# Optimization experiments

Measured on AMD Instinct MI355X. Metric: run time of the kernel, lower is better.

Reference implementation:

```python
import jax, jax.numpy as jnp
import numpy as np

B, N, NIN, NH, NOUT = 32, 64, 256, 256, 2
E = N * (N - 1)
BN_EPS = 1e-5


def _xavier(k, fan_in, fan_out):
    return jax.random.normal(k, (fan_in, fan_out), jnp.float32) * np.sqrt(2.0 / (fan_in + fan_out))


def _mlp_params(key, n_in, n_hid, n_out):
    k1, k2 = jax.random.split(key)
    return {
        'w1': _xavier(k1, n_in, n_hid), 'b1': jnp.full((n_hid,), 0.1, jnp.float32),
        'w2': _xavier(k2, n_hid, n_out), 'b2': jnp.full((n_out,), 0.1, jnp.float32),
        'g': jnp.ones((n_out,), jnp.float32), 'beta': jnp.zeros((n_out,), jnp.float32),
    }


def setup_inputs() -> dict:
    key = jax.random.key(0)
    ks = jax.random.split(key, 7)
    inputs = jax.random.normal(ks[0], (B, N, NIN), jnp.float32)
    # fully-connected directed graph w/o self loops: edge e = (send i, recv j), i != j
    idx = np.array([(i, j) for i in range(N) for j in range(N) if i != j], dtype=np.int64)
    rel_send = np.zeros((E, N), np.float32)
    rel_rec = np.zeros((E, N), np.float32)
    rel_send[np.arange(E), idx[:, 0]] = 1.0
    rel_rec[np.arange(E), idx[:, 1]] = 1.0
    out = {'inputs': inputs, 'rel_rec': jnp.asarray(rel_rec), 'rel_send': jnp.asarray(rel_send)}
    for name, (ni, nh, no), k in [('mlp1', (NIN, NH, NH), ks[1]),
                                  ('mlp2', (2 * NH, NH, NH), ks[2]),
                                  ('mlp3', (NH, NH, NH), ks[3]),
                                  ('mlp4', (3 * NH, NH, NH), ks[4])]:
        p = _mlp_params(k, ni, nh, no)
        for pk, pv in p.items():
            out[f'{name}_{pk}'] = pv
    out['fc_w'] = _xavier(ks[5], NH, NOUT)
    out['fc_b'] = jnp.full((NOUT,), 0.1, jnp.float32)
    return out


def _mlp(x, w1, b1, w2, b2, g, beta):
    # Linear -> ELU -> Linear -> ELU -> BatchNorm1d (training-mode batch stats, biased var)
    h = jax.nn.elu(x @ w1 + b1)
    h = jax.nn.elu(h @ w2 + b2)
    mean = h.mean(axis=(0, 1))
    var = h.var(axis=(0, 1))
    return (h - mean) * jax.lax.rsqrt(var + BN_EPS) * g + beta


def reference(inputs, rel_rec, rel_send,
              mlp1_w1, mlp1_b1, mlp1_w2, mlp1_b2, mlp1_g, mlp1_beta,
              mlp2_w1, mlp2_b1, mlp2_w2, mlp2_b2, mlp2_g, mlp2_beta,
              mlp3_w1, mlp3_b1, mlp3_w2, mlp3_b2, mlp3_g, mlp3_beta,
              mlp4_w1, mlp4_b1, mlp4_w2, mlp4_b2, mlp4_g, mlp4_beta,
              fc_w, fc_b):
    x = _mlp(inputs, mlp1_w1, mlp1_b1, mlp1_w2, mlp1_b2, mlp1_g, mlp1_beta)  # [B,N,NH]
    # node2edge: gather sender/receiver node features per edge
    s = jnp.einsum('en,bnh->beh', rel_send, x)
    r = jnp.einsum('en,bnh->beh', rel_rec, x)
    x = jnp.concatenate([s, r], axis=-1)  # [B,E,2*NH]
    x = _mlp(x, mlp2_w1, mlp2_b1, mlp2_w2, mlp2_b2, mlp2_g, mlp2_beta)
    x_skip = x
    # edge2node: scatter-sum incoming edges per node, normalized by N
    inc = jnp.einsum('en,beh->bnh', rel_rec, x) / N
    x = _mlp(inc, mlp3_w1, mlp3_b1, mlp3_w2, mlp3_b2, mlp3_g, mlp3_beta)
    s = jnp.einsum('en,bnh->beh', rel_send, x)
    r = jnp.einsum('en,bnh->beh', rel_rec, x)
    x = jnp.concatenate([s, r, x_skip], axis=-1)  # [B,E,3*NH]
    x = _mlp(x, mlp4_w1, mlp4_b1, mlp4_w2, mlp4_b2, mlp4_g, mlp4_beta)
    return x @ fc_w + fc_b  # [B,E,NOUT]
```

## Files before the change

kernel.cpp:

```cpp
#include <hip/hip_runtime.h>

typedef __bf16 bf16_t;
typedef __bf16 bf16x8 __attribute__((ext_vector_type(8)));
typedef float  f32x4  __attribute__((ext_vector_type(4)));

#define NB    64
#define EB    4032
#define BATCH 32
#define H     256
#define M_EDGE (BATCH*EB)
#define M_NODE (BATCH*NB)
#define T2    4
#define T4    4
#define BN_EPS 1e-5f

__device__ __forceinline__ void load_lds16(const void* g, void* l) {
    __builtin_amdgcn_global_load_lds(
        (const __attribute__((address_space(1))) unsigned int*)g,
        (__attribute__((address_space(3))) unsigned int*)l, 16, 0, 0);
}
__device__ __forceinline__ float elu(float v) { return v > 0.f ? v : __expf(v) - 1.f; }

template<bool AF32>
__global__ __launch_bounds__(256)
void fused_mlp(const void* __restrict__ A0v,
               const bf16_t* __restrict__ W1t, const float* __restrict__ b1,
               const bf16_t* __restrict__ W2t, const float* __restrict__ b2,
               bf16_t* __restrict__ out, float* __restrict__ stats)
{
    const int m0 = blockIdx.x * 64;
    const int tid = threadIdx.x, wave = tid >> 6, lane = tid & 63;
    const int l15 = lane & 15, quad = lane >> 4;
    const int row = tid >> 2;
    const int cx8 = (((tid & 3) ^ ((tid >> 3) & 3))) * 8;
    const int sl8 = (tid & 3) * 8;
    const int xq8 = (quad ^ ((l15 >> 1) & 3)) * 8;

    __shared__ bf16_t h1s[64 * 264];
    __shared__ bf16_t Bs[256 * 32];
    __shared__ float  sred[512];

    const bf16_t* A0 = (const bf16_t*)A0v;

    f32x4 acc1[4][4];
#pragma unroll
    for (int t = 0; t < 4; ++t)
#pragma unroll
        for (int u = 0; u < 4; ++u) acc1[t][u] = (f32x4){0.f, 0.f, 0.f, 0.f};

    for (int k0 = 0; k0 < 256; k0 += 32) {
        bf16_t* ldsA = h1s + wave * 512;
        if (AF32) {
            const float* af = (const float*)A0v + (size_t)(m0 + row) * 256 + k0 + cx8;
            float4 lo = *(const float4*)af;
            float4 hi = *(const float4*)(af + 4);
            bf16x8 v;
            v[0]=(bf16_t)lo.x; v[1]=(bf16_t)lo.y; v[2]=(bf16_t)lo.z; v[3]=(bf16_t)lo.w;
            v[4]=(bf16_t)hi.x; v[5]=(bf16_t)hi.y; v[6]=(bf16_t)hi.z; v[7]=(bf16_t)hi.w;
            *(bf16x8*)&h1s[row * 32 + sl8] = v;
        } else {
            load_lds16(A0 + (size_t)(m0 + row) * 256 + k0 + cx8, ldsA);
        }
#pragma unroll
        for (int p = 0; p < 4; ++p)
            load_lds16(W1t + (size_t)(p * 64 + row) * 256 + k0 + cx8,
                       Bs + (p * 256 + wave * 64) * 8);
        __syncthreads();
        bf16x8 afr[4], bfr[4];
#pragma unroll
        for (int t = 0; t < 4; ++t)
            afr[t] = *(const bf16x8*)&h1s[(t * 16 + l15) * 32 + xq8];
#pragma unroll
        for (int u = 0; u < 4; ++u)
            bfr[u] = *(const bf16x8*)&Bs[(wave * 64 + u * 16 + l15) * 32 + xq8];
#pragma unroll
        for (int t = 0; t < 4; ++t)
#pragma unroll
            for (int u = 0; u < 4; ++u)
                acc1[t][u] = __builtin_amdgcn_mfma_f32_16x16x32_bf16(afr[t], bfr[u], acc1[t][u], 0, 0, 0);
        __syncthreads();
    }

#pragma unroll
    for (int u = 0; u < 4; ++u) {
        int   col = wave * 64 + u * 16 + l15;
        float bv  = b1[col];
#pragma unroll
        for (int t = 0; t < 4; ++t)
#pragma unroll
            for (int r = 0; r < 4; ++r)
                h1s[(t * 16 + quad * 4 + r) * 264 + col] = (bf16_t)elu(acc1[t][u][r] + bv);
    }
    sred[tid] = 0.f; sred[256 + tid] = 0.f;
    __syncthreads();

    f32x4 acc2[4][4];
#pragma unroll
    for (int t = 0; t < 4; ++t)
#pragma unroll
        for (int u = 0; u < 4; ++u) acc2[t][u] = (f32x4){0.f, 0.f, 0.f, 0.f};

    for (int k0 = 0; k0 < 256; k0 += 32) {
#pragma unroll
        for (int p = 0; p < 4; ++p)
            load_lds16(W2t + (size_t)(p * 64 + row) * 256 + k0 + cx8,
                       Bs + (p * 256 + wave * 64) * 8);
        __syncthreads();
        bf16x8 afr[4], bfr[4];
#pragma unroll
        for (int t = 0; t < 4; ++t)
            afr[t] = *(const bf16x8*)&h1s[(t * 16 + l15) * 264 + k0 + quad * 8];
#pragma unroll
        for (int u = 0; u < 4; ++u)
            bfr[u] = *(const bf16x8*)&Bs[(wave * 64 + u * 16 + l15) * 32 + xq8];
#pragma unroll
        for (int t = 0; t < 4; ++t)
#pragma unroll
            for (int u = 0; u < 4; ++u)
                acc2[t][u] = __builtin_amdgcn_mfma_f32_16x16x32_bf16(afr[t], bfr[u], acc2[t][u], 0, 0, 0);
        __syncthreads();
    }

#pragma unroll
    for (int u = 0; u < 4; ++u) {
        int   col = wave * 64 + u * 16 + l15;
        float bv  = b2[col];
        float s = 0.f, q = 0.f;
#pragma unroll
        for (int t = 0; t < 4; ++t)
#pragma unroll
            for (int r = 0; r < 4; ++r) {
                float v = elu(acc2[t][u][r] + bv);
                h1s[(t * 16 + quad * 4 + r) * 264 + col] = (bf16_t)v;
                s += v; q += v * v;
            }
        s += __shfl_xor(s, 16); s += __shfl_xor(s, 32);
        q += __shfl_xor(q, 16); q += __shfl_xor(q, 32);
        if (quad == 0) { atomicAdd(&sred[col], s); atomicAdd(&sred[256 + col], q); }
    }
    __syncthreads();
#pragma unroll
    for (int p = 0; p < 8; ++p) {
        int idx = p * 256 + tid;
        int r = idx >> 5, ch = idx & 31;
        *(uint4*)&out[(size_t)(m0 + r) * H + ch * 8] = *(const uint4*)&h1s[r * 264 + ch * 8];
    }
    atomicAdd(&stats[tid],     sred[tid]);
    atomicAdd(&stats[H + tid], sred[256 + tid]);
}

__global__ __launch_bounds__(256)
void node_gemm(const bf16_t* __restrict__ A, const float* __restrict__ statsIn,
               const float* __restrict__ g, const float* __restrict__ beta, float Mcnt,
               const bf16_t* __restrict__ Wt, const float* __restrict__ bias,
               float* __restrict__ out)
{
    const int m0 = blockIdx.x * 64;
    const int nb = blockIdx.y * 256;
    const int tid = threadIdx.x, wave = tid >> 6, lane = tid & 63;
    const int l15 = lane & 15, quad = lane >> 4;
    const int row = tid >> 2;
    const int cx8 = (((tid & 3) ^ ((tid >> 3) & 3))) * 8;
    const int sl8 = (tid & 3) * 8;
    const int xq8 = (quad ^ ((l15 >> 1) & 3)) * 8;
    __shared__ bf16_t As[64 * 32];
    __shared__ bf16_t Bs[256 * 32];
    __shared__ float  ss[512];

    {
        float mean = statsIn[tid] / Mcnt;
        float var  = statsIn[256 + tid] / Mcnt - mean * mean;
        float scl  = g[tid] * rsqrtf(var + BN_EPS);
        ss[tid]       = scl;
        ss[256 + tid] = beta[tid] - mean * scl;
    }
    __syncthreads();

    f32x4 acc[4][4];
#pragma unroll
    for (int t = 0; t < 4; ++t)
#pragma unroll
        for (int u = 0; u < 4; ++u) acc[t][u] = (f32x4){0.f, 0.f, 0.f, 0.f};

    for (int k0 = 0; k0 < 256; k0 += 32) {
        {
            int kc = k0 + cx8;
            bf16x8 v = *(const bf16x8*)(A + (size_t)(m0 + row) * 256 + kc);
            bf16x8 w;
#pragma unroll
            for (int j = 0; j < 8; ++j)
                w[j] = (bf16_t)((float)v[j] * ss[kc + j] + ss[256 + kc + j]);
            *(bf16x8*)&As[row * 32 + sl8] = w;
        }
#pragma unroll
        for (int p = 0; p < 4; ++p)
            load_lds16(Wt + (size_t)(nb + p * 64 + row) * 256 + k0 + cx8,
                       Bs + (p * 256 + wave * 64) * 8);
        __syncthreads();
        bf16x8 afr[4], bfr[4];
#pragma unroll
        for (int t = 0; t < 4; ++t)
            afr[t] = *(const bf16x8*)&As[(t * 16 + l15) * 32 + xq8];
#pragma unroll
        for (int u = 0; u < 4; ++u)
            bfr[u] = *(const bf16x8*)&Bs[(wave * 64 + u * 16 + l15) * 32 + xq8];
#pragma unroll
        for (int t = 0; t < 4; ++t)
#pragma unroll
            for (int u = 0; u < 4; ++u)
                acc[t][u] = __builtin_amdgcn_mfma_f32_16x16x32_bf16(afr[t], bfr[u], acc[t][u], 0, 0, 0);
        __syncthreads();
    }
#pragma unroll
    for (int u = 0; u < 4; ++u) {
        int col = nb + wave * 64 + u * 16 + l15;
        float bv = bias[col];
#pragma unroll
        for (int t = 0; t < 4; ++t)
#pragma unroll
            for (int r = 0; r < 4; ++r)
                out[(size_t)(m0 + t * 16 + quad * 4 + r) * 512 + col] = acc[t][u][r] + bv;
    }
}

__global__ __launch_bounds__(256, 2)
void m2_kernel(const float* __restrict__ PQ, const bf16_t* __restrict__ W2t,
               const float* __restrict__ b2, bf16_t* __restrict__ out,
               float* __restrict__ stats)
{
    const int tile0 = blockIdx.x * T2;
    const int tid = threadIdx.x, wave = tid >> 6, lane = tid & 63;
    const int l15 = lane & 15, quad = lane >> 4;

    __shared__ bf16_t Abuf[2][64 * 264];
    __shared__ float  sred[512];

    bf16x8 Breg[32];
#pragma unroll
    for (int ks = 0; ks < 8; ++ks)
#pragma unroll
        for (int u = 0; u < 4; ++u) {
            int col = wave * 64 + u * 16 + l15;
            Breg[ks * 4 + u] = *(const bf16x8*)(W2t + (size_t)col * 256 + ks * 32 + quad * 8);
        }
    sred[tid] = 0.f; sred[256 + tid] = 0.f;

    auto computeA = [&](int t, int b) {
        int row = tid >> 2;
        int m = (tile0 + t) * 64 + row;
        int bb = m / EB, e = m - bb * EB;
        int sn = e / (NB - 1), rr = e - sn * (NB - 1);
        int rc = rr + (rr >= sn ? 1 : 0);
        const float* Prow = PQ + (size_t)(bb * NB + sn) * 512;
        const float* Qrow = PQ + (size_t)(bb * NB + rc) * 512 + 256;
        int c0 = (tid & 3) * 64;
#pragma unroll
        for (int j = 0; j < 8; ++j) {
            int c = c0 + j * 8;
            float4 p0 = *(const float4*)(Prow + c);
            float4 p1 = *(const float4*)(Prow + c + 4);
            float4 q0 = *(const float4*)(Qrow + c);
            float4 q1 = *(const float4*)(Qrow + c + 4);
            bf16x8 v;
            v[0]=(bf16_t)elu(p0.x+q0.x); v[1]=(bf16_t)elu(p0.y+q0.y);
            v[2]=(bf16_t)elu(p0.z+q0.z); v[3]=(bf16_t)elu(p0.w+q0.w);
            v[4]=(bf16_t)elu(p1.x+q1.x); v[5]=(bf16_t)elu(p1.y+q1.y);
            v[6]=(bf16_t)elu(p1.z+q1.z); v[7]=(bf16_t)elu(p1.w+q1.w);
            *(bf16x8*)&Abuf[b][row * 264 + c] = v;
        }
    };

    computeA(0, 0);
    __syncthreads();

    for (int t = 0; t < T2; ++t) {
        const int cur = t & 1, nxt = cur ^ 1;
        if (t + 1 < T2) computeA(t + 1, nxt);

        f32x4 acc[4][4];
#pragma unroll
        for (int a = 0; a < 4; ++a)
#pragma unroll
            for (int u = 0; u < 4; ++u) acc[a][u] = (f32x4){0.f, 0.f, 0.f, 0.f};
#pragma unroll
        for (int ks = 0; ks < 8; ++ks) {
            bf16x8 afr[4];
#pragma unroll
            for (int a = 0; a < 4; ++a)
                afr[a] = *(const bf16x8*)&Abuf[cur][(a * 16 + l15) * 264 + ks * 32 + quad * 8];
#pragma unroll
            for (int a = 0; a < 4; ++a)
#pragma unroll
                for (int u = 0; u < 4; ++u)
                    acc[a][u] = __builtin_amdgcn_mfma_f32_16x16x32_bf16(afr[a], Breg[ks * 4 + u], acc[a][u], 0, 0, 0);
        }
        __syncthreads();

#pragma unroll
        for (int u = 0; u < 4; ++u) {
            int   col = wave * 64 + u * 16 + l15;
            float bv  = b2[col];
            float s = 0.f, q = 0.f;
#pragma unroll
            for (int a = 0; a < 4; ++a)
#pragma unroll
                for (int r = 0; r < 4; ++r) {
                    float v = elu(acc[a][u][r] + bv);
                    Abuf[cur][(a * 16 + quad * 4 + r) * 264 + col] = (bf16_t)v;
                    s += v; q += v * v;
                }
            s += __shfl_xor(s, 16); s += __shfl_xor(s, 32);
            q += __shfl_xor(q, 16); q += __shfl_xor(q, 32);
            if (quad == 0) { atomicAdd(&sred[col], s); atomicAdd(&sred[256 + col], q); }
        }
        __syncthreads();

        size_t m0 = (size_t)(tile0 + t) * 64;
#pragma unroll
        for (int p = 0; p < 8; ++p) {
            int idx = p * 256 + tid;
            int r = idx >> 5, ch = idx & 31;
            *(uint4*)&out[(m0 + r) * H + ch * 8] = *(const uint4*)&Abuf[cur][r * 264 + ch * 8];
        }
        __syncthreads();
    }
    atomicAdd(&stats[tid],     sred[tid]);
    atomicAdd(&stats[H + tid], sred[256 + tid]);
}

__global__ __launch_bounds__(256, 1)
void m4_kernel(const bf16_t* __restrict__ h2, const bf16_t* __restrict__ Wskt,
               const float* __restrict__ RS, const bf16_t* __restrict__ W2t,
               const float* __restrict__ b2, bf16_t* __restrict__ out,
               float* __restrict__ stats)
{
    const int tile0 = blockIdx.x * T4;
    const int tid = threadIdx.x, wave = tid >> 6, lane = tid & 63;
    const int l15 = lane & 15, quad = lane >> 4;

    __shared__ bf16_t Abuf[2][64 * 264];
    __shared__ float  sred[512];

    bf16x8 B1r[32], B2r[32];
#pragma unroll
    for (int ks = 0; ks < 8; ++ks)
#pragma unroll
        for (int u = 0; u < 4; ++u) {
            int col = wave * 64 + u * 16 + l15;
            B1r[ks * 4 + u] = *(const bf16x8*)(Wskt + (size_t)col * 256 + ks * 32 + quad * 8);
            B2r[ks * 4 + u] = *(const bf16x8*)(W2t  + (size_t)col * 256 + ks * 32 + quad * 8);
        }
    sred[tid] = 0.f; sred[256 + tid] = 0.f;

    auto stageA = [&](int t, int b) {
        int row = tid >> 2;
        const bf16_t* src = h2 + ((size_t)(tile0 + t) * 64 + row) * 256;
        int c0 = (tid & 3) * 64;
#pragma unroll
        for (int j = 0; j < 8; ++j) {
            int c = c0 + j * 8;
            *(bf16x8*)&Abuf[b][row * 264 + c] = *(const bf16x8*)(src + c);
        }
    };

    stageA(0, 0);
    __syncthreads();

    for (int t = 0; t < T4; ++t) {
        const int cur = t & 1, nxt = cur ^ 1;
        if (t + 1 < T4) stageA(t + 1, nxt);

        f32x4 acc[4][4];
#pragma unroll
        for (int a = 0; a < 4; ++a)
#pragma unroll
            for (int u = 0; u < 4; ++u) acc[a][u] = (f32x4){0.f, 0.f, 0.f, 0.f};

#pragma unroll
        for (int ks = 0; ks < 8; ++ks) {
            bf16x8 afr[4];
#pragma unroll
            for (int a = 0; a < 4; ++a)
                afr[a] = *(const bf16x8*)&Abuf[cur][(a * 16 + l15) * 264 + ks * 32 + quad * 8];
#pragma unroll
            for (int a = 0; a < 4; ++a)
#pragma unroll
                for (int u = 0; u < 4; ++u)
                    acc[a][u] = __builtin_amdgcn_mfma_f32_16x16x32_bf16(afr[a], B1r[ks * 4 + u], acc[a][u], 0, 0, 0);
        }
        __syncthreads();

#pragma unroll
        for (int u = 0; u < 4; ++u) {
            int col = wave * 64 + u * 16 + l15;
#pragma unroll
            for (int a = 0; a < 4; ++a)
#pragma unroll
                for (int r = 0; r < 4; ++r)
                    Abuf[cur][(a * 16 + quad * 4 + r) * 264 + col] = (bf16_t)acc[a][u][r];
        }
        __syncthreads();

        {
            int row = tid >> 2;
            int m = (tile0 + t) * 64 + row;
            int bb = m / EB, e = m - bb * EB;
            int sn = e / (NB - 1), rr = e - sn * (NB - 1);
            int rc = rr + (rr >= sn ? 1 : 0);
            const float* Srow = RS + (size_t)(bb * NB + sn) * 512;
            const float* Rrow = RS + (size_t)(bb * NB + rc) * 512 + 256;
            int c0 = (tid & 3) * 64;
#pragma unroll
            for (int j = 0; j < 8; ++j) {
                int c = c0 + j * 8;
                bf16x8 h = *(const bf16x8*)&Abuf[cur][row * 264 + c];
                float4 s0 = *(const float4*)(Srow + c);
                float4 s1 = *(const float4*)(Srow + c + 4);
                float4 r0 = *(const float4*)(Rrow + c);
                float4 r1 = *(const float4*)(Rrow + c + 4);
                bf16x8 v;
                v[0]=(bf16_t)elu((float)h[0]+s0.x+r0.x); v[1]=(bf16_t)elu((float)h[1]+s0.y+r0.y);
                v[2]=(bf16_t)elu((float)h[2]+s0.z+r0.z); v[3]=(bf16_t)elu((float)h[3]+s0.w+r0.w);
                v[4]=(bf16_t)elu((float)h[4]+s1.x+r1.x); v[5]=(bf16_t)elu((float)h[5]+s1.y+r1.y);
                v[6]=(bf16_t)elu((float)h[6]+s1.z+r1.z); v[7]=(bf16_t)elu((float)h[7]+s1.w+r1.w);
                *(bf16x8*)&Abuf[cur][row * 264 + c] = v;
            }
        }
        __syncthreads();

#pragma unroll
        for (int a = 0; a < 4; ++a)
#pragma unroll
            for (int u = 0; u < 4; ++u) acc[a][u] = (f32x4){0.f, 0.f, 0.f, 0.f};
#pragma unroll
        for (int ks = 0; ks < 8; ++ks) {
            bf16x8 afr[4];
#pragma unroll
            for (int a = 0; a < 4; ++a)
                afr[a] = *(const bf16x8*)&Abuf[cur][(a * 16 + l15) * 264 + ks * 32 + quad * 8];
#pragma unroll
            for (int a = 0; a < 4; ++a)
#pragma unroll
                for (int u = 0; u < 4; ++u)
                    acc[a][u] = __builtin_amdgcn_mfma_f32_16x16x32_bf16(afr[a], B2r[ks * 4 + u], acc[a][u], 0, 0, 0);
        }
        __syncthreads();

#pragma unroll
        for (int u = 0; u < 4; ++u) {
            int   col = wave * 64 + u * 16 + l15;
            float bv  = b2[col];
            float s = 0.f, q = 0.f;
#pragma unroll
            for (int a = 0; a < 4; ++a)
#pragma unroll
                for (int r = 0; r < 4; ++r) {
                    float v = elu(acc[a][u][r] + bv);
                    Abuf[cur][(a * 16 + quad * 4 + r) * 264 + col] = (bf16_t)v;
                    s += v; q += v * v;
                }
            s += __shfl_xor(s, 16); s += __shfl_xor(s, 32);
            q += __shfl_xor(q, 16); q += __shfl_xor(q, 32);
            if (quad == 0) { atomicAdd(&sred[col], s); atomicAdd(&sred[256 + col], q); }
        }
        __syncthreads();

        size_t m0 = (size_t)(tile0 + t) * 64;
#pragma unroll
        for (int p = 0; p < 8; ++p) {
            int idx = p * 256 + tid;
            int r = idx >> 5, ch = idx & 31;
            *(uint4*)&out[(m0 + r) * H + ch * 8] = *(const uint4*)&Abuf[cur][r * 264 + ch * 8];
        }
        __syncthreads();
    }
    atomicAdd(&stats[tid],     sred[tid]);
    atomicAdd(&stats[H + tid], sred[256 + tid]);
}

__global__ void prep(const float* __restrict__ w1a, bf16_t* __restrict__ wt1a,
                     const float* __restrict__ w1b, bf16_t* __restrict__ wt1b,
                     const float* __restrict__ w2b, bf16_t* __restrict__ wt2b,
                     const float* __restrict__ w3a, bf16_t* __restrict__ wt3a,
                     const float* __restrict__ w3b, bf16_t* __restrict__ wt3b,
                     const float* __restrict__ w4b, bf16_t* __restrict__ wt4b,
                     const float* __restrict__ w2a, bf16_t* __restrict__ wtpq,
                     const float* __restrict__ w4a, bf16_t* __restrict__ wtrs,
                     const float* __restrict__ b2a, float* __restrict__ biasPQ,
                     float* __restrict__ stats)
{
    int blk = blockIdx.x, tid = threadIdx.x;
    if (blk < 1536) {
        int grp = blk >> 8, lb = blk & 255;
        const float* w; bf16_t* wt;
        switch (grp) {
            case 0: w = w1a; wt = wt1a; break;
            case 1: w = w1b; wt = wt1b; break;
            case 2: w = w2b; wt = wt2b; break;
            case 3: w = w3a; wt = wt3a; break;
            case 4: w = w3b; wt = wt3b; break;
            default: w = w4b; wt = wt4b; break;
        }
        int idx = lb * 256 + tid;
        int k = idx >> 8, n = idx & 255;
        wt[n * 256 + k] = (bf16_t)w[idx];
    } else if (blk < 2560) {
        int lb = blk - 1536;
        const float* w = (lb < 512) ? w2a : w4a;
        bf16_t* wt = (lb < 512) ? wtpq : wtrs;
        int c = lb & 511, k = tid;
        float v = (c < 256) ? w[k * 256 + c] : w[(256 + k) * 256 + (c - 256)];
        wt[c * 256 + k] = (bf16_t)v;
    } else if (blk == 2560) {
        biasPQ[tid] = b2a[tid];
        biasPQ[256 + tid] = 0.f;
    } else {
        for (int j = 0; j < 8; ++j) stats[j * 256 + tid] = 0.f;
    }
}

__global__ void prep2(const float* __restrict__ w4a, const float* __restrict__ stats2,
                      const float* __restrict__ g2, const float* __restrict__ be2,
                      const float* __restrict__ b4a, bf16_t* __restrict__ wt,
                      float* __restrict__ bias)
{
    __shared__ float sh2s[256];
    int blk = blockIdx.x, tid = threadIdx.x;
    float mean = stats2[tid] / (float)M_EDGE;
    float var  = stats2[256 + tid] / (float)M_EDGE - mean * mean;
    float scl  = g2[tid] * rsqrtf(var + BN_EPS);
    if (blk < 256) {
        wt[blk * 256 + tid] = (bf16_t)(w4a[(512 + tid) * 256 + blk] * scl);
    } else {
        sh2s[tid] = be2[tid] - mean * scl;
        __syncthreads();
        float acc = 0.f;
        for (int k = 0; k < 256; ++k)
            acc += sh2s[k] * w4a[(512 + k) * 256 + tid];
        bias[tid] = b4a[tid] + acc;
        bias[256 + tid] = 0.f;
    }
}

__global__ void edge2node(const bf16_t* __restrict__ x2, const float* __restrict__ stats2,
                          const float* __restrict__ g2, const float* __restrict__ be2,
                          bf16_t* __restrict__ inc)
{
    int bn = blockIdx.x, bb = bn >> 6, n = bn & 63;
    int g = threadIdx.x >> 5, t = threadIdx.x & 31;
    __shared__ float part[8][256];
    __shared__ float ss[512];
    {
        int c = threadIdx.x;
        float mean = stats2[c] / (float)M_EDGE;
        float var  = stats2[256 + c] / (float)M_EDGE - mean * mean;
        float scl  = g2[c] * rsqrtf(var + BN_EPS);
        ss[c]       = scl;
        ss[256 + c] = be2[c] - mean * scl;
    }
    const bf16_t* base = x2 + (size_t)bb * EB * H;
    float a[8] = {0.f,0.f,0.f,0.f,0.f,0.f,0.f,0.f};
    for (int i = g; i < NB; i += 8) {
        if (i == n) continue;
        int e = i * (NB - 1) + n - (n > i ? 1 : 0);
        bf16x8 v = *(const bf16x8*)&base[(size_t)e * H + t * 8];
#pragma unroll
        for (int j = 0; j < 8; ++j) a[j] += (float)v[j];
    }
#pragma unroll
    for (int j = 0; j < 8; ++j) part[g][t * 8 + j] = a[j];
    __syncthreads();
    int c = threadIdx.x;
    float s = 0.f;
#pragma unroll
    for (int g2i = 0; g2i < 8; ++g2i) s += part[g2i][c];
    inc[(size_t)bn * H + c] = (bf16_t)(s * (1.f / 64.f) * ss[c] + ss[256 + c] * (63.f / 64.f));
}

__global__ void fc_kernel(const bf16_t* __restrict__ x4, const float* __restrict__ stats4,
                          const float* __restrict__ g4, const float* __restrict__ be4,
                          const float* __restrict__ fcw, const float* __restrict__ fcb,
                          float* __restrict__ out)
{
    __shared__ float ss[512];
    {
        int c = threadIdx.x;
        float mean = stats4[c] / (float)M_EDGE;
        float var  = stats4[256 + c] / (float)M_EDGE - mean * mean;
        float scl  = g4[c] * rsqrtf(var + BN_EPS);
        ss[c]       = scl;
        ss[256 + c] = be4[c] - mean * scl;
    }
    __syncthreads();
    int row  = blockIdx.x * 8 + (threadIdx.x >> 5);
    int t    = threadIdx.x & 31;
    bf16x8 v8 = *(const bf16x8*)(x4 + (size_t)row * H + t * 8);
    float s0 = 0.f, s1 = 0.f;
#pragma unroll
    for (int j = 0; j < 8; ++j) {
        int c = t * 8 + j;
        float v = (float)v8[j] * ss[c] + ss[256 + c];
        s0 += v * fcw[c * 2];
        s1 += v * fcw[c * 2 + 1];
    }
#pragma unroll
    for (int off = 16; off; off >>= 1) {
        s0 += __shfl_down(s0, off, 32);
        s1 += __shfl_down(s1, off, 32);
    }
    if (t == 0) {
        out[(size_t)row * 2]     = s0 + fcb[0];
        out[(size_t)row * 2 + 1] = s1 + fcb[1];
    }
}

extern "C" void kernel_launch(void* const* d_in, const int* in_sizes, int n_in,
                              void* d_out, int out_size, void* d_ws, size_t ws_size,
                              hipStream_t stream)
{
    (void)in_sizes; (void)n_in; (void)out_size; (void)ws_size;
    const float* inp = (const float*)d_in[0];
    const float* w1a = (const float*)d_in[3];  const float* b1a = (const float*)d_in[4];
    const float* w1b = (const float*)d_in[5];  const float* b1b = (const float*)d_in[6];
    const float* g1  = (const float*)d_in[7];  const float* be1 = (const float*)d_in[8];
    const float* w2a = (const float*)d_in[9];  const float* b2a = (const float*)d_in[10];
    const float* w2b = (const float*)d_in[11]; const float* b2b = (const float*)d_in[12];
    const float* g2  = (const float*)d_in[13]; const float* be2 = (const float*)d_in[14];
    const float* w3a = (const float*)d_in[15]; const float* b3a = (const float*)d_in[16];
    const float* w3b = (const float*)d_in[17]; const float* b3b = (const float*)d_in[18];
    const float* g3  = (const float*)d_in[19]; const float* be3 = (const float*)d_in[20];
    const float* w4a = (const float*)d_in[21]; const float* b4a = (const float*)d_in[22];
    const float* w4b = (const float*)d_in[23]; const float* b4b = (const float*)d_in[24];
    const float* g4  = (const float*)d_in[25]; const float* be4 = (const float*)d_in[26];
    const float* fcw = (const float*)d_in[27]; const float* fcb = (const float*)d_in[28];

    char* p = (char*)d_ws;
    auto alloc = [&](size_t nbytes) { char* r = p; p += (nbytes + 255) & ~(size_t)255; return r; };

    bf16_t* wt1a = (bf16_t*)alloc(256 * 256 * 2);
    bf16_t* wt1b = (bf16_t*)alloc(256 * 256 * 2);
    bf16_t* wt2b = (bf16_t*)alloc(256 * 256 * 2);
    bf16_t* wt3a = (bf16_t*)alloc(256 * 256 * 2);
    bf16_t* wt3b = (bf16_t*)alloc(256 * 256 * 2);
    bf16_t* wt4b = (bf16_t*)alloc(256 * 256 * 2);
    bf16_t* wtpq = (bf16_t*)alloc(512 * 256 * 2);
    bf16_t* wtrs = (bf16_t*)alloc(512 * 256 * 2);
    bf16_t* wtsk = (bf16_t*)alloc(256 * 256 * 2);
    float*  biasPQ = (float*)alloc(512 * sizeof(float));
    float*  biasRS = (float*)alloc(512 * sizeof(float));
    float*  stats  = (float*)alloc(4 * 512 * sizeof(float));
    bf16_t* x1   = (bf16_t*)alloc((size_t)M_NODE * H * 2);
    bf16_t* incb = (bf16_t*)alloc((size_t)M_NODE * H * 2);
    bf16_t* x3   = (bf16_t*)alloc((size_t)M_NODE * H * 2);
    float*  PQ   = (float*)alloc((size_t)M_NODE * 512 * sizeof(float));
    float*  RS   = (float*)alloc((size_t)M_NODE * 512 * sizeof(float));
    bf16_t* h2   = (bf16_t*)alloc((size_t)M_EDGE * H * 2);
    bf16_t* h4   = (bf16_t*)alloc((size_t)M_EDGE * H * 2);

    prep<<<2562, 256, 0, stream>>>(w1a, wt1a, w1b, wt1b, w2b, wt2b, w3a, wt3a,
                                   w3b, wt3b, w4b, wt4b, w2a, wtpq, w4a, wtrs,
                                   b2a, biasPQ, stats);

    fused_mlp<true ><<<M_NODE / 64, 256, 0, stream>>>(inp, wt1a, b1a, wt1b, b1b, x1, stats + 0);

    { dim3 g(M_NODE / 64, 2);
      node_gemm<<<g, 256, 0, stream>>>(x1, stats + 0, g1, be1, (float)M_NODE, wtpq, biasPQ, PQ); }

    m2_kernel<<<M_EDGE / (64 * T2), 256, 0, stream>>>(PQ, wt2b, b2b, h2, stats + 512);

    edge2node<<<M_NODE, 256, 0, stream>>>(h2, stats + 512, g2, be2, incb);
    fused_mlp<false><<<M_NODE / 64, 256, 0, stream>>>(incb, wt3a, b3a, wt3b, b3b, x3, stats + 1024);

    prep2<<<257, 256, 0, stream>>>(w4a, stats + 512, g2, be2, b4a, wtsk, biasRS);
    { dim3 g(M_NODE / 64, 2);
      node_gemm<<<g, 256, 0, stream>>>(x3, stats + 1024, g3, be3, (float)M_NODE, wtrs, biasRS, RS); }

    m4_kernel<<<M_EDGE / (64 * T4), 256, 0, stream>>>(h2, wtsk, RS, wt4b, b4b, h4, stats + 1536);

    fc_kernel<<<M_EDGE / 8, 256, 0, stream>>>(h4, stats + 1536, g4, be4, fcw, fcb, (float*)d_out);
}
```

Before: 408.8 us.

## Restructure m4 kernel to one tile per block for two blocks per CU

The m4 kernel now handles a single 64-row tile per block instead of looping over four tiles with double-buffered LDS. One register array holds the weights and is reloaded with the second-layer weights between the two GEMMs, which halves register use. The LDS buffer shrinks to a single tile, and launch bounds now ask for two blocks per CU. The aim is more resident waves to hide latency. In exchange, weights are reloaded per tile, there is no prefetch overlap of the next tile, and four times as many blocks issue global stats atomics.

```diff
diff --git a/kernel.cpp b/kernel.cpp
--- a/kernel.cpp
+++ b/kernel.cpp
@@ -11,7 +11,6 @@
 #define M_EDGE (BATCH*EB)
 #define M_NODE (BATCH*NB)
 #define T2    4
-#define T4    4
 #define BN_EPS 1e-5f
 
 __device__ __forceinline__ void load_lds16(const void* g, void* l) {
@@ -328,151 +327,147 @@
     atomicAdd(&stats[H + tid], sred[256 + tid]);
 }
 
-__global__ __launch_bounds__(256, 1)
+__global__ __launch_bounds__(256, 2)
 void m4_kernel(const bf16_t* __restrict__ h2, const bf16_t* __restrict__ Wskt,
                const float* __restrict__ RS, const bf16_t* __restrict__ W2t,
                const float* __restrict__ b2, bf16_t* __restrict__ out,
                float* __restrict__ stats)
 {
-    const int tile0 = blockIdx.x * T4;
+    const int m0 = blockIdx.x * 64;
     const int tid = threadIdx.x, wave = tid >> 6, lane = tid & 63;
     const int l15 = lane & 15, quad = lane >> 4;
-
-    __shared__ bf16_t Abuf[2][64 * 264];
+    const int row = tid >> 2;
+    const int c0 = (tid & 3) * 64;
+
+    __shared__ bf16_t h1s[64 * 264];
     __shared__ float  sred[512];
 
-    bf16x8 B1r[32], B2r[32];
+    bf16x8 Breg[32];
 #pragma unroll
     for (int ks = 0; ks < 8; ++ks)
 #pragma unroll
         for (int u = 0; u < 4; ++u) {
             int col = wave * 64 + u * 16 + l15;
-            B1r[ks * 4 + u] = *(const bf16x8*)(Wskt + (size_t)col * 256 + ks * 32 + quad * 8);
-            B2r[ks * 4 + u] = *(const bf16x8*)(W2t  + (size_t)col * 256 + ks * 32 + quad * 8);
+            Breg[ks * 4 + u] = *(const bf16x8*)(Wskt + (size_t)col * 256 + ks * 32 + quad * 8);
         }
     sred[tid] = 0.f; sred[256 + tid] = 0.f;
 
-    auto stageA = [&](int t, int b) {
-        int row = tid >> 2;
-        const bf16_t* src = h2 + ((size_t)(tile0 + t) * 64 + row) * 256;
-        int c0 = (tid & 3) * 64;
+    {
+        const bf16_t* src = h2 + (size_t)(m0 + row) * 256;
 #pragma unroll
         for (int j = 0; j < 8; ++j) {
             int c = c0 + j * 8;
-            *(bf16x8*)&Abuf[b][row * 264 + c] = *(const bf16x8*)(src + c);
-        }
-    };
-
-    stageA(0, 0);
-    __syncthreads();
-
-    for (int t = 0; t < T4; ++t) {
-        const int cur = t & 1, nxt = cur ^ 1;
-        if (t + 1 < T4) stageA(t + 1, nxt);
-
-        f32x4 acc[4][4];
+            *(bf16x8*)&h1s[row * 264 + c] = *(const bf16x8*)(src + c);
+        }
+    }
+    __syncthreads();
+
+    f32x4 acc[4][4];
+#pragma unroll
+    for (int a = 0; a < 4; ++a)
+#pragma unroll
+        for (int u = 0; u < 4; ++u) acc[a][u] = (f32x4){0.f, 0.f, 0.f, 0.f};
+
+#pragma unroll
+    for (int ks = 0; ks < 8; ++ks) {
+        bf16x8 afr[4];
 #pragma unroll
         for (int a = 0; a < 4; ++a)
-#pragma unroll
-            for (int u = 0; u < 4; ++u) acc[a][u] = (f32x4){0.f, 0.f, 0.f, 0.f};
-
-#pragma unroll
-        for (int ks = 0; ks < 8; ++ks) {
-            bf16x8 afr[4];
-#pragma unroll
-            for (int a = 0; a < 4; ++a)
-                afr[a] = *(const bf16x8*)&Abuf[cur][(a * 16 + l15) * 264 + ks * 32 + quad * 8];
-#pragma unroll
-            for (int a = 0; a < 4; ++a)
-#pragma unroll
-                for (int u = 0; u < 4; ++u)
-                    acc[a][u] = __builtin_amdgcn_mfma_f32_16x16x32_bf16(afr[a], B1r[ks * 4 + u], acc[a][u], 0, 0, 0);
-        }
-        __syncthreads();
-
+            afr[a] = *(const bf16x8*)&h1s[(a * 16 + l15) * 264 + ks * 32 + quad * 8];
+#pragma unroll
+        for (int a = 0; a < 4; ++a)
+#pragma unroll
+            for (int u = 0; u < 4; ++u)
+                acc[a][u] = __builtin_amdgcn_mfma_f32_16x16x32_bf16(afr[a], Breg[ks * 4 + u], acc[a][u], 0, 0, 0);
+    }
+
+#pragma unroll
+    for (int ks = 0; ks < 8; ++ks)
 #pragma unroll
         for (int u = 0; u < 4; ++u) {
             int col = wave * 64 + u * 16 + l15;
-#pragma unroll
-            for (int a = 0; a < 4; ++a)
-#pragma unroll
-                for (int r = 0; r < 4; ++r)
-                    Abuf[cur][(a * 16 + quad * 4 + r) * 264 + col] = (bf16_t)acc[a][u][r];
-        }
-        __syncthreads();
-
-        {
-            int row = tid >> 2;
-            int m = (tile0 + t) * 64 + row;
-            int bb = m / EB, e = m - bb * EB;
-            int sn = e / (NB - 1), rr = e - sn * (NB - 1);
-            int rc = rr + (rr >= sn ? 1 : 0);
-            const float* Srow = RS + (size_t)(bb * NB + sn) * 512;
-            const float* Rrow = RS + (size_t)(bb * NB + rc) * 512 + 256;
-            int c0 = (tid & 3) * 64;
-#pragma unroll
-            for (int j = 0; j < 8; ++j) {
-                int c = c0 + j * 8;
-                bf16x8 h = *(const bf16x8*)&Abuf[cur][row * 264 + c];
-                float4 s0 = *(const float4*)(Srow + c);
-                float4 s1 = *(const float4*)(Srow + c + 4);
-                float4 r0 = *(const float4*)(Rrow + c);
-                float4 r1 = *(const float4*)(Rrow + c + 4);
-                bf16x8 v;
-                v[0]=(bf16_t)elu((float)h[0]+s0.x+r0.x); v[1]=(bf16_t)elu((float)h[1]+s0.y+r0.y);
-                v[2]=(bf16_t)elu((float)h[2]+s0.z+r0.z); v[3]=(bf16_t)elu((float)h[3]+s0.w+r0.w);
-                v[4]=(bf16_t)elu((float)h[4]+s1.x+r1.x); v[5]=(bf16_t)elu((float)h[5]+s1.y+r1.y);
-                v[6]=(bf16_t)elu((float)h[6]+s1.z+r1.z); v[7]=(bf16_t)elu((float)h[7]+s1.w+r1.w);
-                *(bf16x8*)&Abuf[cur][row * 264 + c] = v;
+            Breg[ks * 4 + u] = *(const bf16x8*)(W2t + (size_t)col * 256 + ks * 32 + quad * 8);
+        }
+    __syncthreads();
+
+#pragma unroll
+    for (int u = 0; u < 4; ++u) {
+        int col = wave * 64 + u * 16 + l15;
+#pragma unroll
+        for (int a = 0; a < 4; ++a)
+#pragma unroll
+            for (int r = 0; r < 4; ++r)
+                h1s[(a * 16 + quad * 4 + r) * 264 + col] = (bf16_t)acc[a][u][r];
+    }
+    __syncthreads();
+
+    {
+        int m = m0 + row;
+        int bb = m / EB, e = m - bb * EB;
+        int sn = e / (NB - 1), rr = e - sn * (NB - 1);
+        int rc = rr + (rr >= sn ? 1 : 0);
+        const float* Srow = RS + (size_t)(bb * NB + sn) * 512;
+        const float* Rrow = RS + (size_t)(bb * NB + rc) * 512 + 256;
+#pragma unroll
+        for (int j = 0; j < 8; ++j) {
+            int c = c0 + j * 8;
+            bf16x8 h = *(const bf16x8*)&h1s[row * 264 + c];
+            float4 s0 = *(const float4*)(Srow + c);
+            float4 s1 = *(const float4*)(Srow + c + 4);
+            float4 r0 = *(const float4*)(Rrow + c);
+            float4 r1 = *(const float4*)(Rrow + c + 4);
+            bf16x8 v;
+            v[0]=(bf16_t)elu((float)h[0]+s0.x+r0.x); v[1]=(bf16_t)elu((float)h[1]+s0.y+r0.y);
+            v[2]=(bf16_t)elu((float)h[2]+s0.z+r0.z); v[3]=(bf16_t)elu((float)h[3]+s0.w+r0.w);
+            v[4]=(bf16_t)elu((float)h[4]+s1.x+r1.x); v[5]=(bf16_t)elu((float)h[5]+s1.y+r1.y);
+            v[6]=(bf16_t)elu((float)h[6]+s1.z+r1.z); v[7]=(bf16_t)elu((float)h[7]+s1.w+r1.w);
+            *(bf16x8*)&h1s[row * 264 + c] = v;
+        }
+    }
+    __syncthreads();
+
+#pragma unroll
+    for (int a = 0; a < 4; ++a)
+#pragma unroll
+        for (int u = 0; u < 4; ++u) acc[a][u] = (f32x4){0.f, 0.f, 0.f, 0.f};
+#pragma unroll
+    for (int ks = 0; ks < 8; ++ks) {
+        bf16x8 afr[4];
+#pragma unroll
+        for (int a = 0; a < 4; ++a)
+            afr[a] = *(const bf16x8*)&h1s[(a * 16 + l15) * 264 + ks * 32 + quad * 8];
+#pragma unroll
+        for (int a = 0; a < 4; ++a)
+#pragma unroll
+            for (int u = 0; u < 4; ++u)
+                acc[a][u] = __builtin_amdgcn_mfma_f32_16x16x32_bf16(afr[a], Breg[ks * 4 + u], acc[a][u], 0, 0, 0);
+    }
+    __syncthreads();
+
+#pragma unroll
+    for (int u = 0; u < 4; ++u) {
+        int   col = wave * 64 + u * 16 + l15;
+        float bv  = b2[col];
+        float s = 0.f, q = 0.f;
+#pragma unroll
+        for (int a = 0; a < 4; ++a)
+#pragma unroll
+            for (int r = 0; r < 4; ++r) {
+                float v = elu(acc[a][u][r] + bv);
+                h1s[(a * 16 + quad * 4 + r) * 264 + col] = (bf16_t)v;
+                s += v; q += v * v;
             }
-        }
-        __syncthreads();
-
-#pragma unroll
-        for (int a = 0; a < 4; ++a)
-#pragma unroll
-            for (int u = 0; u < 4; ++u) acc[a][u] = (f32x4){0.f, 0.f, 0.f, 0.f};
-#pragma unroll
-        for (int ks = 0; ks < 8; ++ks) {
-            bf16x8 afr[4];
-#pragma unroll
-            for (int a = 0; a < 4; ++a)
-                afr[a] = *(const bf16x8*)&Abuf[cur][(a * 16 + l15) * 264 + ks * 32 + quad * 8];
-#pragma unroll
-            for (int a = 0; a < 4; ++a)
-#pragma unroll
-                for (int u = 0; u < 4; ++u)
-                    acc[a][u] = __builtin_amdgcn_mfma_f32_16x16x32_bf16(afr[a], B2r[ks * 4 + u], acc[a][u], 0, 0, 0);
-        }
-        __syncthreads();
-
-#pragma unroll
-        for (int u = 0; u < 4; ++u) {
-            int   col = wave * 64 + u * 16 + l15;
-            float bv  = b2[col];
-            float s = 0.f, q = 0.f;
-#pragma unroll
-            for (int a = 0; a < 4; ++a)
-#pragma unroll
-                for (int r = 0; r < 4; ++r) {
-                    float v = elu(acc[a][u][r] + bv);
-                    Abuf[cur][(a * 16 + quad * 4 + r) * 264 + col] = (bf16_t)v;
-                    s += v; q += v * v;
-                }
-            s += __shfl_xor(s, 16); s += __shfl_xor(s, 32);
-            q += __shfl_xor(q, 16); q += __shfl_xor(q, 32);
-            if (quad == 0) { atomicAdd(&sred[col], s); atomicAdd(&sred[256 + col], q); }
-        }
-        __syncthreads();
-
-        size_t m0 = (size_t)(tile0 + t) * 64;
-#pragma unroll
-        for (int p = 0; p < 8; ++p) {
-            int idx = p * 256 + tid;
-            int r = idx >> 5, ch = idx & 31;
-            *(uint4*)&out[(m0 + r) * H + ch * 8] = *(const uint4*)&Abuf[cur][r * 264 + ch * 8];
-        }
-        __syncthreads();
+        s += __shfl_xor(s, 16); s += __shfl_xor(s, 32);
+        q += __shfl_xor(q, 16); q += __shfl_xor(q, 32);
+        if (quad == 0) { atomicAdd(&sred[col], s); atomicAdd(&sred[256 + col], q); }
+    }
+    __syncthreads();
+
+#pragma unroll
+    for (int p = 0; p < 8; ++p) {
+        int idx = p * 256 + tid;
+        int r = idx >> 5, ch = idx & 31;
+        *(uint4*)&out[(size_t)(m0 + r) * H + ch * 8] = *(const uint4*)&h1s[r * 264 + ch * 8];
     }
     atomicAdd(&stats[tid],     sred[tid]);
     atomicAdd(&stats[H + tid], sred[256 + tid]);
@@ -675,7 +670,7 @@
     { dim3 g(M_NODE / 64, 2);
       node_gemm<<<g, 256, 0, stream>>>(x3, stats + 1024, g3, be3, (float)M_NODE, wtrs, biasRS, RS); }
 
-    m4_kernel<<<M_EDGE / (64 * T4), 256, 0, stream>>>(h2, wtsk, RS, wt4b, b4b, h4, stats + 1536);
+    m4_kernel<<<M_EDGE / 64, 256, 0, stream>>>(h2, wtsk, RS, wt4b, b4b, h4, stats + 1536);
 
     fc_kernel<<<M_EDGE / 8, 256, 0, stream>>>(h4, stats + 1536, g4, be4, fcw, fcb, (float*)d_out);
 }
```

After: 394.6 us. 3.5% less time.
